# Kernel tuning notes

Measured on AMD Instinct MI355X. Metric: run time of the kernel, lower is better.

## Reference

```python
import jax, jax.numpy as jnp
import numpy as np

B, P, O, C = 32, 65536, 32, 2
THRESH = 0.35
VAR = (0.1, 0.2)
LOC_W, LANDM_W = 2.0, 1.0
ALPHA, GAMMA = 0.25, 1.5
EPS = 1e-7


def setup_inputs():
    key = jax.random.key(0)
    k = jax.random.split(key, 8)
    loc_data = jax.random.normal(k[0], (B, P, 4), jnp.float32) * 0.1
    conf_data = jax.random.normal(k[1], (B, P, C), jnp.float32)
    landm_data = jax.random.normal(k[2], (B, P, 10), jnp.float32) * 0.1
    # priors in center form (cx, cy, w, h)
    cxcy = jax.random.uniform(k[3], (P, 2), minval=0.05, maxval=0.95)
    wh = jax.random.uniform(k[4], (P, 2), minval=0.02, maxval=0.3)
    priors = jnp.concatenate([cxcy, wh], axis=-1).astype(jnp.float32)
    # targets [B, O, 15]: corner box (4) + 5 landmarks (10) + label (1, in {-1, +1})
    xy1 = jax.random.uniform(k[5], (B, O, 2), minval=0.0, maxval=0.7)
    bwh = jax.random.uniform(k[6], (B, O, 2), minval=0.05, maxval=0.25)
    boxes = jnp.concatenate([xy1, xy1 + bwh], axis=-1)
    landms = jnp.tile(xy1 + bwh * 0.5, (1, 1, 5))
    labels = (jax.random.randint(k[7], (B, O, 1), 0, 2) * 2 - 1).astype(jnp.float32)
    targets = jnp.concatenate([boxes, landms, labels], axis=-1)
    return {"loc_data": loc_data, "conf_data": conf_data, "landm_data": landm_data,
            "priors": priors, "targets": targets}


def point_form(pr):  # (cx,cy,w,h) -> (x1,y1,x2,y2)
    return jnp.concatenate([pr[:, :2] - pr[:, 2:] / 2, pr[:, :2] + pr[:, 2:] / 2], -1)


def pairwise_iou(a, b):  # a [O,4], b [P,4] corner form -> [O,P]
    lt = jnp.maximum(a[:, None, :2], b[None, :, :2])
    rb = jnp.minimum(a[:, None, 2:], b[None, :, 2:])
    whd = jnp.clip(rb - lt, 0.0)
    inter = whd[..., 0] * whd[..., 1]
    area_a = ((a[:, 2] - a[:, 0]) * (a[:, 3] - a[:, 1]))[:, None]
    area_b = ((b[:, 2] - b[:, 0]) * (b[:, 3] - b[:, 1]))[None, :]
    return inter / (area_a + area_b - inter)


def encode_landm(matched, priors):  # matched [P,10], priors [P,4] center form
    m = matched.reshape(P, 5, 2)
    g = (m - priors[:, None, :2]) / (VAR[0] * priors[:, None, 2:])
    return g.reshape(P, 10)


def match_one(truths, landms, labels, priors_pf, priors):
    ov = pairwise_iou(truths, priors_pf)                       # [O,P]
    best_prior_idx = jnp.argmax(ov, axis=1)                    # [O] best prior per gt
    best_truth_overlap = ov.max(axis=0)                        # [P]
    best_truth_idx = jnp.argmax(ov, axis=0)                    # [P]
    # ensure every gt keeps its best prior
    best_truth_overlap = best_truth_overlap.at[best_prior_idx].set(2.0)
    best_truth_idx = best_truth_idx.at[best_prior_idx].set(jnp.arange(truths.shape[0]))
    loc_t = truths[best_truth_idx]                             # [P,4] matched gt boxes (corner)
    conf = jnp.where(best_truth_overlap < THRESH, 0.0, labels[best_truth_idx])
    landm_t = encode_landm(landms[best_truth_idx], priors)     # [P,10]
    return loc_t, conf, landm_t


def decode(loc, priors):  # SSD center-form decode -> corner boxes
    xy = priors[..., :2] + loc[..., :2] * VAR[0] * priors[..., 2:]
    wh = priors[..., 2:] * jnp.exp(loc[..., 2:] * VAR[1])
    return jnp.concatenate([xy - wh / 2, xy + wh / 2], -1)


def giou(b1, b2):  # elementwise GIoU, corner form
    area1 = (b1[..., 2] - b1[..., 0]) * (b1[..., 3] - b1[..., 1])
    area2 = (b2[..., 2] - b2[..., 0]) * (b2[..., 3] - b2[..., 1])
    iw = jnp.clip(jnp.minimum(b1[..., 2], b2[..., 2]) - jnp.maximum(b1[..., 0], b2[..., 0]), 0.0)
    ih = jnp.clip(jnp.minimum(b1[..., 3], b2[..., 3]) - jnp.maximum(b1[..., 1], b2[..., 1]), 0.0)
    inter = iw * ih
    union = area1 + area2 - inter
    iou = inter / (union + EPS)
    ew = jnp.maximum(b1[..., 2], b2[..., 2]) - jnp.minimum(b1[..., 0], b2[..., 0])
    eh = jnp.maximum(b1[..., 3], b2[..., 3]) - jnp.minimum(b1[..., 1], b2[..., 1])
    enc = ew * eh
    return iou - (enc - union) / (enc + EPS)


def smooth_l1(x):
    ax = jnp.abs(x)
    return jnp.where(ax < 1.0, 0.5 * x * x, ax - 0.5)


def reference(loc_data, conf_data, landm_data, priors, targets):
    # matching uses detached (.data) priors/targets in the original
    priors_c = jax.lax.stop_gradient(priors)
    targets_c = jax.lax.stop_gradient(targets)
    truths, landms, labels = targets_c[..., :4], targets_c[..., 4:14], targets_c[..., 14]
    priors_pf = point_form(priors_c)
    loc_t, conf_raw, landm_t = jax.vmap(match_one, in_axes=(0, 0, 0, None, None))(
        truths, landms, labels, priors_pf, priors_c)  # [B,P,4],[B,P],[B,P,10]

    # landmark loss on pos1 = conf > 0 (label +1: face with landmarks)
    pos1 = conf_raw > 0
    N1 = jnp.maximum(pos1.sum().astype(jnp.float32), 1.0)
    loss_landm = (smooth_l1(landm_data - landm_t).sum(-1) * pos1).sum() * LANDM_W

    # loc GIoU loss on pos = conf != 0
    pos = conf_raw != 0
    conf_t = pos.astype(jnp.int32)  # conf_t[pos] = 1, background 0
    dec = decode(loc_data, priors_c[None])  # [B,P,4]
    loss_l = jnp.where(pos, 1.0 - giou(dec, loc_t), 0.0).sum() * LOC_W

    # focal loss over all B*P anchors (size_average=False -> sum)
    logp = jax.nn.log_softmax(conf_data, axis=-1)
    logp_t = jnp.take_along_axis(logp, conf_t[..., None], axis=-1)[..., 0]
    p_t = jnp.exp(logp_t)
    loss_c = (-ALPHA * (1.0 - p_t) ** GAMMA * logp_t).sum()

    # original normalizes loss_l and loss_c by num_pos_landm sum (N), landm by N1 (==N)
    N = N1
    return (loss_l / N, loss_c / N, loss_landm / N1)
```

## Files before the change

### kernel.cpp

```cpp
#include <hip/hip_runtime.h>
#include <cstdint>

#define B_ 32
#define P_ 65536
#define O_ 32
#define GX_ 64
#define KC_ 4
#define NCELL_ 16
#define NC_ (NCELL_ * NCELL_)
#define HB_ 32
#define PPH_ (P_ / (HB_ * 256))
#define MARGIN_ 0.1501f
#define THRESH_ 0.35f
#define VAR0 0.1f
#define VAR1 0.2f
#define EPS_ 1e-7f
#define ALPHA_ 0.25f

struct WSHdr {
  unsigned long long gkey[B_ * O_];
  float4 part[GX_ * B_];
  double corr[B_][4];
  unsigned blkcnt[HB_ * NC_];
  unsigned blkbase[HB_ * NC_];
  unsigned cellid[P_];
  unsigned idx_sorted[P_];
  float4 priors_sorted[P_];
};

__device__ __forceinline__ float frcp(float x) { return __builtin_amdgcn_rcpf(x); }

template <int CTRL>
__device__ __forceinline__ float dpp_fmax(float v) {
  int s = __builtin_amdgcn_update_dpp(0, __float_as_int(v), CTRL, 0xF, 0xF, true);
  return fmaxf(v, __int_as_float(s));
}
template <int CTRL>
__device__ __forceinline__ unsigned dpp_umax(unsigned v) {
  unsigned u = (unsigned)__builtin_amdgcn_update_dpp(0, (int)v, CTRL, 0xF, 0xF, true);
  return u > v ? u : v;
}

__device__ __forceinline__ float focal_term(float2 cf, bool pos) {
  float mx = fmaxf(cf.x, cf.y);
  float lse = mx + __logf(1.f + __expf(-fabsf(cf.x - cf.y)));
  float logpt = (pos ? cf.y : cf.x) - lse;
  float pt = __expf(logpt);
  float om = 1.f - pt;
  return -ALPHA_ * om * sqrtf(om) * logpt;
}

__device__ __forceinline__ float giou_term(float4 pr, float4 loc,
                                           float b2x1, float b2y1,
                                           float b2x2, float b2y2) {
  float dx = pr.x + loc.x * VAR0 * pr.z;
  float dy = pr.y + loc.y * VAR0 * pr.w;
  float dw = pr.z * __expf(loc.z * VAR1);
  float dh = pr.w * __expf(loc.w * VAR1);
  float b1x1 = dx - dw * 0.5f, b1y1 = dy - dh * 0.5f;
  float b1x2 = dx + dw * 0.5f, b1y2 = dy + dh * 0.5f;
  float a1 = (b1x2 - b1x1) * (b1y2 - b1y1);
  float a2 = (b2x2 - b2x1) * (b2y2 - b2y1);
  float iw = fmaxf(fminf(b1x2, b2x2) - fmaxf(b1x1, b2x1), 0.f);
  float ih = fmaxf(fminf(b1y2, b2y2) - fmaxf(b1y1, b2y1), 0.f);
  float inter = iw * ih;
  float uni = a1 + a2 - inter;
  float iou = inter * frcp(uni + EPS_);
  float ew = fmaxf(b1x2, b2x2) - fminf(b1x1, b2x1);
  float eh = fmaxf(b1y2, b2y2) - fminf(b1y1, b2y1);
  float enc = ew * eh;
  float g = iou - (enc - uni) * frcp(enc + EPS_);
  return 1.f - g;
}

__device__ __forceinline__ float landm_term(float4 pr,
                                            const float* __restrict__ lmrow,
                                            const float* __restrict__ tlm_row) {
  float rw = frcp(VAR0 * pr.z);
  float rh = frcp(VAR0 * pr.w);
  float llm = 0.f;
  #pragma unroll
  for (int q = 0; q < 5; ++q) {
    float2 d = *reinterpret_cast<const float2*>(lmrow + q * 2);
    float ex = d.x - (tlm_row[2 * q] - pr.x) * rw;
    float ey = d.y - (tlm_row[2 * q + 1] - pr.y) * rh;
    float ax = fabsf(ex), ay = fabsf(ey);
    llm += (ax < 1.f) ? 0.5f * ex * ex : ax - 0.5f;
    llm += (ay < 1.f) ? 0.5f * ey * ey : ay - 0.5f;
  }
  return llm;
}


__global__ __launch_bounds__(256) void k_init2(WSHdr* ws) {
  const int t = blockIdx.x * 256 + threadIdx.x;
  if (t < B_ * O_) ws->gkey[t] = 0xFFFFFFFFull;
}

__global__ __launch_bounds__(256) void k_hist(const float* __restrict__ priors,
                                              WSHdr* __restrict__ ws) {
  __shared__ unsigned lh[NC_];
  const int tid = threadIdx.x;
  lh[tid] = 0u;
  __syncthreads();
  const int pb0 = blockIdx.x * (256 * PPH_);
  #pragma unroll
  for (int i = 0; i < PPH_; ++i) {
    const int p = pb0 + i * 256 + tid;
    float4 pr = reinterpret_cast<const float4*>(priors)[p];
    int cx = min(NCELL_ - 1, max(0, (int)(pr.x * (float)NCELL_)));
    int cy = min(NCELL_ - 1, max(0, (int)(pr.y * (float)NCELL_)));
    unsigned c = (unsigned)(cy * NCELL_ + cx);
    ws->cellid[p] = c;
    atomicAdd(&lh[c], 1u);
  }
  __syncthreads();
  ws->blkcnt[blockIdx.x * NC_ + tid] = lh[tid];
}

__global__ __launch_bounds__(256) void k_scan2(WSHdr* ws) {
  __shared__ unsigned s[NC_];
  const int c = threadIdx.x;
  unsigned tot = 0;
  for (int blk = 0; blk < HB_; ++blk) tot += ws->blkcnt[blk * NC_ + c];
  s[c] = tot;
  __syncthreads();
  for (int off = 1; off < NC_; off <<= 1) {
    unsigned t = (c >= off) ? s[c - off] : 0u;
    __syncthreads();
    s[c] += t;
    __syncthreads();
  }
  unsigned run = s[c] - tot;
  for (int blk = 0; blk < HB_; ++blk) {
    ws->blkbase[blk * NC_ + c] = run;
    run += ws->blkcnt[blk * NC_ + c];
  }
}

__global__ __launch_bounds__(256) void k_scatter2(const float* __restrict__ priors,
                                                  WSHdr* __restrict__ ws) {
  __shared__ unsigned lcur[NC_];
  const int tid = threadIdx.x;
  lcur[tid] = ws->blkbase[blockIdx.x * NC_ + tid];
  __syncthreads();
  const int pb0 = blockIdx.x * (256 * PPH_);
  #pragma unroll
  for (int i = 0; i < PPH_; ++i) {
    const int p = pb0 + i * 256 + tid;
    unsigned c = ws->cellid[p];
    unsigned slot = atomicAdd(&lcur[c], 1u);
    ws->idx_sorted[slot] = (unsigned)p;
    ws->priors_sorted[slot] = reinterpret_cast<const float4*>(priors)[p];
  }
}

__global__ __launch_bounds__(256) void k_fused2(const float* __restrict__ loc_data,
                                                const float* __restrict__ conf_data,
                                                const float* __restrict__ landm_data,
                                                const float* __restrict__ targets,
                                                WSHdr* __restrict__ ws) {
  __shared__ float tsh[O_][4];
  __shared__ float tlbl[O_];
  __shared__ float tlm[O_][10];
  __shared__ unsigned long long kq[O_][17];
  __shared__ float4 wsum[4];
  const int b = blockIdx.y;
  const int tid = threadIdx.x;
  const int lane = tid & 63, wid = tid >> 6;
  if (tid < O_) {
    const float* trow = targets + ((size_t)b * O_ + tid) * 15;
    tsh[tid][0] = trow[0]; tsh[tid][1] = trow[1];
    tsh[tid][2] = trow[2]; tsh[tid][3] = trow[3];
    #pragma unroll
    for (int k = 0; k < 10; ++k) tlm[tid][k] = trow[4 + k];
    tlbl[tid] = trow[14];
  }
  for (int i = tid; i < O_ * 17; i += 256) ((unsigned long long*)kq)[i] = 0ull;
  __syncthreads();

  const int slot0 = blockIdx.x * 1024 + tid * KC_;
  float4 pr[KC_];
  float px1[KC_], py1[KC_], px2[KC_], py2[KC_], pa[KC_], bov[KC_];
  int bidx[KC_];
  unsigned pinv[KC_];
  uint4 opv = *reinterpret_cast<const uint4*>(&ws->idx_sorted[slot0]);
  pinv[0] = 0xFFFFFFFFu - opv.x; pinv[1] = 0xFFFFFFFFu - opv.y;
  pinv[2] = 0xFFFFFFFFu - opv.z; pinv[3] = 0xFFFFFFFFu - opv.w;
  float mnx = 1e9f, mxx = -1e9f, mny = 1e9f, mxy = -1e9f;
  #pragma unroll
  for (int k = 0; k < KC_; ++k) {
    pr[k] = ws->priors_sorted[slot0 + k];
    px1[k] = pr[k].x - pr[k].z * 0.5f; py1[k] = pr[k].y - pr[k].w * 0.5f;
    px2[k] = pr[k].x + pr[k].z * 0.5f; py2[k] = pr[k].y + pr[k].w * 0.5f;
    pa[k] = (px2[k] - px1[k]) * (py2[k] - py1[k]);
    bov[k] = 0.f; bidx[k] = 0;
    mnx = fminf(mnx, pr[k].x); mxx = fmaxf(mxx, pr[k].x);
    mny = fminf(mny, pr[k].y); mxy = fmaxf(mxy, pr[k].y);
  }
  #pragma unroll
  for (int i = 1; i < 64; i <<= 1) {
    mnx = fminf(mnx, __shfl_xor(mnx, i));
    mxx = fmaxf(mxx, __shfl_xor(mxx, i));
    mny = fminf(mny, __shfl_xor(mny, i));
    mxy = fmaxf(mxy, __shfl_xor(mxy, i));
  }

  const float* __restrict__ tb = targets + (size_t)b * O_ * 15;
  for (int o = 0; o < O_; ++o) {
    const float x1 = tb[o * 15 + 0], y1 = tb[o * 15 + 1];
    const float x2 = tb[o * 15 + 2], y2 = tb[o * 15 + 3];
    bool hit = (x1 - MARGIN_ <= mxx) && (x2 + MARGIN_ >= mnx) &&
               (y1 - MARGIN_ <= mxy) && (y2 + MARGIN_ >= mny);
    if (hit) {
      const float ta = (x2 - x1) * (y2 - y1);
      float tiou = 0.f;
      unsigned tinv = 0u;
      #pragma unroll
      for (int k = 0; k < KC_; ++k) {
        float iw = fmaxf(fminf(x2, px2[k]) - fmaxf(x1, px1[k]), 0.f);
        float ih = fmaxf(fminf(y2, py2[k]) - fmaxf(y1, py1[k]), 0.f);
        float inter = iw * ih;
        float iou = inter * frcp(ta + pa[k] - inter);
        if (iou > bov[k]) { bov[k] = iou; bidx[k] = o; }
        if (iou > tiou || (iou == tiou && pinv[k] > tinv)) {
          tiou = iou; tinv = pinv[k];
        }
      }
      float m = tiou;
      m = dpp_fmax<0x128>(m);
      m = dpp_fmax<0x124>(m);
      m = dpp_fmax<0x122>(m);
      m = dpp_fmax<0x121>(m);
      unsigned cand = (tiou == m) ? tinv : 0u;
      cand = dpp_umax<0x128>(cand);
      cand = dpp_umax<0x124>(cand);
      cand = dpp_umax<0x122>(cand);
      cand = dpp_umax<0x121>(cand);
      if ((lane & 15) == 0)
        kq[o][wid * 4 + (lane >> 4)] =
            ((unsigned long long)__float_as_uint(m) << 32) |
            (unsigned long long)cand;
    }
  }

  float vx = 0.f, vy = 0.f, vz = 0.f, vw = 0.f;
  #pragma unroll
  for (int k = 0; k < KC_; ++k) {
    const unsigned p = 0xFFFFFFFFu - pinv[k];
    const size_t bp = (size_t)b * P_ + p;
    const float ov = bov[k];
    const int idx = bidx[k];
    const bool pos = !(ov < THRESH_);
    const bool pos1 = pos && (tlbl[idx] > 0.f);
    float2 cf = reinterpret_cast<const float2*>(conf_data)[bp];
    vy += focal_term(cf, pos);
    if (pos) {
      float4 loc = reinterpret_cast<const float4*>(loc_data)[bp];
      vx += giou_term(pr[k], loc, tsh[idx][0], tsh[idx][1], tsh[idx][2], tsh[idx][3]);
      if (pos1) {
        vw += 1.f;
        vz += landm_term(pr[k], landm_data + bp * 10, &tlm[idx][0]);
      }
    }
  }

  __syncthreads();
  if (tid < O_) {
    unsigned long long best = kq[tid][0];
    #pragma unroll
    for (int s = 1; s < 16; ++s) {
      unsigned long long v = kq[tid][s];
      if (v > best) best = v;
    }
    atomicMax(&ws->gkey[(size_t)b * O_ + tid], best);
  }

  #pragma unroll
  for (int i = 32; i > 0; i >>= 1) {
    vx += __shfl_xor(vx, i);
    vy += __shfl_xor(vy, i);
    vz += __shfl_xor(vz, i);
    vw += __shfl_xor(vw, i);
  }
  if (lane == 0) wsum[wid] = make_float4(vx, vy, vz, vw);
  __syncthreads();
  if (tid == 0) {
    float sx = 0.f, sy = 0.f, sz = 0.f, sw = 0.f;
    #pragma unroll
    for (int w = 0; w < 4; ++w) {
      sx += wsum[w].x; sy += wsum[w].y; sz += wsum[w].z; sw += wsum[w].w;
    }
    ws->part[(size_t)blockIdx.y * GX_ + blockIdx.x] = make_float4(sx, sy, sz, sw);
  }
}

__global__ __launch_bounds__(64) void k_fix(const float* __restrict__ loc_data,
                                            const float* __restrict__ conf_data,
                                            const float* __restrict__ landm_data,
                                            const float* __restrict__ priors,
                                            const float* __restrict__ targets,
                                            WSHdr* __restrict__ ws) {
  __shared__ float tsh[O_][5];
  __shared__ float tlbl[O_];
  __shared__ float tlm[O_][10];
  const int b = blockIdx.x;
  const int tid = threadIdx.x;
  if (tid < O_) {
    const float* trow = targets + ((size_t)b * O_ + tid) * 15;
    float x1 = trow[0], y1 = trow[1], x2 = trow[2], y2 = trow[3];
    tsh[tid][0] = x1; tsh[tid][1] = y1; tsh[tid][2] = x2; tsh[tid][3] = y2;
    tsh[tid][4] = (x2 - x1) * (y2 - y1);
    #pragma unroll
    for (int k = 0; k < 10; ++k) tlm[tid][k] = trow[4 + k];
    tlbl[tid] = trow[14];
  }
  __syncthreads();

  unsigned fp = 0xFFFFFFFFu;
  if (tid < O_)
    fp = 0xFFFFFFFFu - (unsigned)(ws->gkey[(size_t)b * O_ + tid] & 0xFFFFFFFFull);
  bool alive = tid < O_;
  for (int j2 = 0; j2 < O_; ++j2) {
    unsigned f2 = __shfl(fp, j2, 64);
    if (j2 > tid && f2 == fp) alive = false;
  }

  float dll = 0.f, dlc = 0.f, dllm = 0.f, dn1 = 0.f;
  if (alive) {
    const int p = (int)fp;
    const size_t bp = (size_t)b * P_ + p;
    float4 pr = reinterpret_cast<const float4*>(priors)[p];
    float px1 = pr.x - pr.z * 0.5f, py1 = pr.y - pr.w * 0.5f;
    float px2 = pr.x + pr.z * 0.5f, py2 = pr.y + pr.w * 0.5f;
    float pa = (px2 - px1) * (py2 - py1);
    float bov = 0.f;
    int bidx = 0;
    for (int o = 0; o < O_; ++o) {
      const float x1 = tsh[o][0], y1 = tsh[o][1], x2 = tsh[o][2], y2 = tsh[o][3];
      const float ta = tsh[o][4];
      float iw = fmaxf(fminf(x2, px2) - fmaxf(x1, px1), 0.f);
      float ih = fmaxf(fminf(y2, py2) - fmaxf(y1, py1), 0.f);
      float inter = iw * ih;
      float iou = inter * frcp(ta + pa - inter);
      if (iou > bov) { bov = iou; bidx = o; }
    }
    float2 cf = reinterpret_cast<const float2*>(conf_data)[bp];
    float4 loc = reinterpret_cast<const float4*>(loc_data)[bp];
    const float* lmrow = landm_data + bp * 10;
    {
      const bool pos = !(bov < THRESH_);
      const bool pos1 = pos && (tlbl[bidx] > 0.f);
      dlc -= focal_term(cf, pos);
      if (pos) {
        dll -= giou_term(pr, loc, tsh[bidx][0], tsh[bidx][1], tsh[bidx][2], tsh[bidx][3]);
        if (pos1) {
          dn1 -= 1.f;
          dllm -= landm_term(pr, lmrow, &tlm[bidx][0]);
        }
      }
    }
    {
      const int idx = tid;
      const bool pos1 = tlbl[idx] > 0.f;
      dlc += focal_term(cf, true);
      dll += giou_term(pr, loc, tsh[idx][0], tsh[idx][1], tsh[idx][2], tsh[idx][3]);
      if (pos1) {
        dn1 += 1.f;
        dllm += landm_term(pr, lmrow, &tlm[idx][0]);
      }
    }
  }
  #pragma unroll
  for (int i = 32; i > 0; i >>= 1) {
    dll += __shfl_xor(dll, i);
    dlc += __shfl_xor(dlc, i);
    dllm += __shfl_xor(dllm, i);
    dn1 += __shfl_xor(dn1, i);
  }
  if (tid == 0) {
    ws->corr[b][0] = (double)dll;
    ws->corr[b][1] = (double)dlc;
    ws->corr[b][2] = (double)dllm;
    ws->corr[b][3] = (double)dn1;
  }
}

__global__ __launch_bounds__(256) void k_final(const WSHdr* __restrict__ ws,
                                               float* __restrict__ out) {
  __shared__ double sh[4][4];
  const int tid = threadIdx.x;
  double sx = 0.0, sy = 0.0, sz = 0.0, sw = 0.0;
  for (int i = tid; i < GX_ * B_; i += 256) {
    float4 v = ws->part[i];
    sx += v.x; sy += v.y; sz += v.z; sw += v.w;
  }
  if (tid < B_) {
    sx += ws->corr[tid][0];
    sy += ws->corr[tid][1];
    sz += ws->corr[tid][2];
    sw += ws->corr[tid][3];
  }
  #pragma unroll
  for (int i = 32; i > 0; i >>= 1) {
    sx += __shfl_xor(sx, i);
    sy += __shfl_xor(sy, i);
    sz += __shfl_xor(sz, i);
    sw += __shfl_xor(sw, i);
  }
  const int wave = tid >> 6, lane = tid & 63;
  if (lane == 0) { sh[wave][0] = sx; sh[wave][1] = sy; sh[wave][2] = sz; sh[wave][3] = sw; }
  __syncthreads();
  if (tid == 0) {
    double ax = 0, ay = 0, az = 0, aw = 0;
    #pragma unroll
    for (int w = 0; w < 4; ++w) { ax += sh[w][0]; ay += sh[w][1]; az += sh[w][2]; aw += sh[w][3]; }
    double n1 = aw < 1.0 ? 1.0 : aw;
    out[0] = (float)(2.0 * ax / n1);
    out[1] = (float)(ay / n1);
    out[2] = (float)(az / n1);
  }
}

extern "C" void kernel_launch(void* const* d_in, const int* in_sizes, int n_in,
                              void* d_out, int out_size, void* d_ws, size_t ws_size,
                              hipStream_t stream) {
  (void)in_sizes; (void)n_in; (void)out_size; (void)ws_size;
  const float* loc     = (const float*)d_in[0];
  const float* conf    = (const float*)d_in[1];
  const float* landm   = (const float*)d_in[2];
  const float* priors  = (const float*)d_in[3];
  const float* targets = (const float*)d_in[4];
  WSHdr* ws = (WSHdr*)d_ws;
  float* out = (float*)d_out;

  hipLaunchKernelGGL(k_init2, dim3(4), dim3(256), 0, stream, ws);
  hipLaunchKernelGGL(k_hist, dim3(HB_), dim3(256), 0, stream, priors, ws);
  hipLaunchKernelGGL(k_scan2, dim3(1), dim3(256), 0, stream, ws);
  hipLaunchKernelGGL(k_scatter2, dim3(HB_), dim3(256), 0, stream, priors, ws);
  hipLaunchKernelGGL(k_fused2, dim3(GX_, B_), dim3(256), 0, stream,
                     loc, conf, landm, targets, ws);
  hipLaunchKernelGGL(k_fix, dim3(B_), dim3(64), 0, stream,
                     loc, conf, landm, priors, targets, ws);
  hipLaunchKernelGGL(k_final, dim3(1), dim3(256), 0, stream, ws, out);
}
```

Measured before the change: 88.12 us.

## Split fused match/loss kernel so loss reads inputs in original coalesced order

The fused matching-and-loss kernel is split in two. The matching kernel now writes per-prior best IoU and index, packed into 32 bits, in sorted order. A new loss kernel walks priors in their original order, finding each result through a sortrank table, so the large loc, conf and landmark reads become coalesced instead of scattered gathers. The init kernel is folded into the histogram kernel to save a launch. The cost is an extra launch plus a B*P intermediate buffer that is written and read back, and the packing truncates the low 6 IoU bits.

Result: slower. 105.2 us (+19.3%).

```diff
diff --git a/kernel.cpp b/kernel.cpp
--- a/kernel.cpp
+++ b/kernel.cpp
@@ -23,8 +23,8 @@
   double corr[B_][4];
   unsigned blkcnt[HB_ * NC_];
   unsigned blkbase[HB_ * NC_];
-  unsigned cellid[P_];
   unsigned idx_sorted[P_];
+  unsigned sortrank[P_];
   float4 priors_sorted[P_];
 };
 
@@ -92,16 +92,15 @@
 }
 
 
-__global__ __launch_bounds__(256) void k_init2(WSHdr* ws) {
-  const int t = blockIdx.x * 256 + threadIdx.x;
-  if (t < B_ * O_) ws->gkey[t] = 0xFFFFFFFFull;
-}
-
 __global__ __launch_bounds__(256) void k_hist(const float* __restrict__ priors,
-                                              WSHdr* __restrict__ ws) {
+                                              WSHdr* __restrict__ ws,
+                                              unsigned* __restrict__ cellid) {
   __shared__ unsigned lh[NC_];
   const int tid = threadIdx.x;
   lh[tid] = 0u;
+  if (blockIdx.x == 0) {
+    for (int i = tid; i < B_ * O_; i += 256) ws->gkey[i] = 0xFFFFFFFFull;
+  }
   __syncthreads();
   const int pb0 = blockIdx.x * (256 * PPH_);
   #pragma unroll
@@ -111,7 +110,7 @@
     int cx = min(NCELL_ - 1, max(0, (int)(pr.x * (float)NCELL_)));
     int cy = min(NCELL_ - 1, max(0, (int)(pr.y * (float)NCELL_)));
     unsigned c = (unsigned)(cy * NCELL_ + cx);
-    ws->cellid[p] = c;
+    cellid[p] = c;
     atomicAdd(&lh[c], 1u);
   }
   __syncthreads();
@@ -139,7 +138,8 @@
 }
 
 __global__ __launch_bounds__(256) void k_scatter2(const float* __restrict__ priors,
-                                                  WSHdr* __restrict__ ws) {
+                                                  WSHdr* __restrict__ ws,
+                                                  const unsigned* __restrict__ cellid) {
   __shared__ unsigned lcur[NC_];
   const int tid = threadIdx.x;
   lcur[tid] = ws->blkbase[blockIdx.x * NC_ + tid];
@@ -148,39 +148,24 @@
   #pragma unroll
   for (int i = 0; i < PPH_; ++i) {
     const int p = pb0 + i * 256 + tid;
-    unsigned c = ws->cellid[p];
+    unsigned c = cellid[p];
     unsigned slot = atomicAdd(&lcur[c], 1u);
     ws->idx_sorted[slot] = (unsigned)p;
+    ws->sortrank[p] = slot;
     ws->priors_sorted[slot] = reinterpret_cast<const float4*>(priors)[p];
   }
 }
 
-__global__ __launch_bounds__(256) void k_fused2(const float* __restrict__ loc_data,
-                                                const float* __restrict__ conf_data,
-                                                const float* __restrict__ landm_data,
-                                                const float* __restrict__ targets,
-                                                WSHdr* __restrict__ ws) {
-  __shared__ float tsh[O_][4];
-  __shared__ float tlbl[O_];
-  __shared__ float tlm[O_][10];
+__global__ __launch_bounds__(256) void k_match2(const float* __restrict__ targets,
+                                                WSHdr* __restrict__ ws,
+                                                unsigned* __restrict__ pb32) {
   __shared__ unsigned long long kq[O_][17];
-  __shared__ float4 wsum[4];
   const int b = blockIdx.y;
   const int tid = threadIdx.x;
   const int lane = tid & 63, wid = tid >> 6;
-  if (tid < O_) {
-    const float* trow = targets + ((size_t)b * O_ + tid) * 15;
-    tsh[tid][0] = trow[0]; tsh[tid][1] = trow[1];
-    tsh[tid][2] = trow[2]; tsh[tid][3] = trow[3];
-    #pragma unroll
-    for (int k = 0; k < 10; ++k) tlm[tid][k] = trow[4 + k];
-    tlbl[tid] = trow[14];
-  }
   for (int i = tid; i < O_ * 17; i += 256) ((unsigned long long*)kq)[i] = 0ull;
-  __syncthreads();
 
   const int slot0 = blockIdx.x * 1024 + tid * KC_;
-  float4 pr[KC_];
   float px1[KC_], py1[KC_], px2[KC_], py2[KC_], pa[KC_], bov[KC_];
   int bidx[KC_];
   unsigned pinv[KC_];
@@ -190,13 +175,13 @@
   float mnx = 1e9f, mxx = -1e9f, mny = 1e9f, mxy = -1e9f;
   #pragma unroll
   for (int k = 0; k < KC_; ++k) {
-    pr[k] = ws->priors_sorted[slot0 + k];
-    px1[k] = pr[k].x - pr[k].z * 0.5f; py1[k] = pr[k].y - pr[k].w * 0.5f;
-    px2[k] = pr[k].x + pr[k].z * 0.5f; py2[k] = pr[k].y + pr[k].w * 0.5f;
+    float4 pr = ws->priors_sorted[slot0 + k];
+    px1[k] = pr.x - pr.z * 0.5f; py1[k] = pr.y - pr.w * 0.5f;
+    px2[k] = pr.x + pr.z * 0.5f; py2[k] = pr.y + pr.w * 0.5f;
     pa[k] = (px2[k] - px1[k]) * (py2[k] - py1[k]);
     bov[k] = 0.f; bidx[k] = 0;
-    mnx = fminf(mnx, pr[k].x); mxx = fmaxf(mxx, pr[k].x);
-    mny = fminf(mny, pr[k].y); mxy = fmaxf(mxy, pr[k].y);
+    mnx = fminf(mnx, pr.x); mxx = fmaxf(mxx, pr.x);
+    mny = fminf(mny, pr.y); mxy = fmaxf(mxy, pr.y);
   }
   #pragma unroll
   for (int i = 1; i < 64; i <<= 1) {
@@ -205,6 +190,7 @@
     mny = fminf(mny, __shfl_xor(mny, i));
     mxy = fmaxf(mxy, __shfl_xor(mxy, i));
   }
+  __syncthreads();
 
   const float* __restrict__ tb = targets + (size_t)b * O_ * 15;
   for (int o = 0; o < O_; ++o) {
@@ -244,26 +230,12 @@
     }
   }
 
-  float vx = 0.f, vy = 0.f, vz = 0.f, vw = 0.f;
-  #pragma unroll
-  for (int k = 0; k < KC_; ++k) {
-    const unsigned p = 0xFFFFFFFFu - pinv[k];
-    const size_t bp = (size_t)b * P_ + p;
-    const float ov = bov[k];
-    const int idx = bidx[k];
-    const bool pos = !(ov < THRESH_);
-    const bool pos1 = pos && (tlbl[idx] > 0.f);
-    float2 cf = reinterpret_cast<const float2*>(conf_data)[bp];
-    vy += focal_term(cf, pos);
-    if (pos) {
-      float4 loc = reinterpret_cast<const float4*>(loc_data)[bp];
-      vx += giou_term(pr[k], loc, tsh[idx][0], tsh[idx][1], tsh[idx][2], tsh[idx][3]);
-      if (pos1) {
-        vw += 1.f;
-        vz += landm_term(pr[k], landm_data + bp * 10, &tlm[idx][0]);
-      }
-    }
-  }
+  uint4 outv;
+  outv.x = (__float_as_uint(bov[0]) & 0xFFFFFFC0u) | (unsigned)bidx[0];
+  outv.y = (__float_as_uint(bov[1]) & 0xFFFFFFC0u) | (unsigned)bidx[1];
+  outv.z = (__float_as_uint(bov[2]) & 0xFFFFFFC0u) | (unsigned)bidx[2];
+  outv.w = (__float_as_uint(bov[3]) & 0xFFFFFFC0u) | (unsigned)bidx[3];
+  *reinterpret_cast<uint4*>(&pb32[(size_t)b * P_ + slot0]) = outv;
 
   __syncthreads();
   if (tid < O_) {
@@ -275,6 +247,53 @@
     }
     atomicMax(&ws->gkey[(size_t)b * O_ + tid], best);
   }
+}
+
+__global__ __launch_bounds__(256) void k_loss3(const float* __restrict__ loc_data,
+                                               const float* __restrict__ conf_data,
+                                               const float* __restrict__ landm_data,
+                                               const float* __restrict__ priors,
+                                               const float* __restrict__ targets,
+                                               WSHdr* __restrict__ ws,
+                                               const unsigned* __restrict__ pb32) {
+  __shared__ float tx1[O_], ty1[O_], tx2[O_], ty2[O_], tlbl[O_];
+  __shared__ float tlm[O_][10];
+  __shared__ float4 wsum[4];
+  const int b = blockIdx.y;
+  const int tid = threadIdx.x;
+  if (tid < O_) {
+    const float* trow = targets + ((size_t)b * O_ + tid) * 15;
+    tx1[tid] = trow[0]; ty1[tid] = trow[1]; tx2[tid] = trow[2]; ty2[tid] = trow[3];
+    #pragma unroll
+    for (int k = 0; k < 10; ++k) tlm[tid][k] = trow[4 + k];
+    tlbl[tid] = trow[14];
+  }
+  __syncthreads();
+
+  float vx = 0.f, vy = 0.f, vz = 0.f, vw = 0.f;
+  #pragma unroll
+  for (int k = 0; k < KC_; ++k) {
+    const unsigned p = (unsigned)((blockIdx.x * KC_ + k) * 256 + tid);
+    const size_t bp = (size_t)b * P_ + p;
+    const unsigned slot = ws->sortrank[p];
+    const unsigned v = pb32[(size_t)b * P_ + slot];
+    const float ov = __uint_as_float(v & 0xFFFFFFC0u);
+    const int idx = (int)(v & 0x3Fu);
+    const bool pos = !(ov < THRESH_);
+    const bool pos1 = pos && (tlbl[idx] > 0.f);
+
+    float2 cf = reinterpret_cast<const float2*>(conf_data)[bp];
+    vy += focal_term(cf, pos);
+    if (pos) {
+      float4 pr = reinterpret_cast<const float4*>(priors)[p];
+      float4 loc = reinterpret_cast<const float4*>(loc_data)[bp];
+      vx += giou_term(pr, loc, tx1[idx], ty1[idx], tx2[idx], ty2[idx]);
+      if (pos1) {
+        vw += 1.f;
+        vz += landm_term(pr, landm_data + bp * 10, &tlm[idx][0]);
+      }
+    }
+  }
 
   #pragma unroll
   for (int i = 32; i > 0; i >>= 1) {
@@ -283,7 +302,8 @@
     vz += __shfl_xor(vz, i);
     vw += __shfl_xor(vw, i);
   }
-  if (lane == 0) wsum[wid] = make_float4(vx, vy, vz, vw);
+  const int wave = tid >> 6, lane = tid & 63;
+  if (lane == 0) wsum[wave] = make_float4(vx, vy, vz, vw);
   __syncthreads();
   if (tid == 0) {
     float sx = 0.f, sy = 0.f, sz = 0.f, sw = 0.f;
@@ -349,7 +369,8 @@
     float4 loc = reinterpret_cast<const float4*>(loc_data)[bp];
     const float* lmrow = landm_data + bp * 10;
     {
-      const bool pos = !(bov < THRESH_);
+      const float ovt = __uint_as_float(__float_as_uint(bov) & 0xFFFFFFC0u);
+      const bool pos = !(ovt < THRESH_);
       const bool pos1 = pos && (tlbl[bidx] > 0.f);
       dlc -= focal_term(cf, pos);
       if (pos) {
@@ -432,14 +453,16 @@
   const float* priors  = (const float*)d_in[3];
   const float* targets = (const float*)d_in[4];
   WSHdr* ws = (WSHdr*)d_ws;
+  unsigned* aux = (unsigned*)((char*)d_ws + sizeof(WSHdr));
   float* out = (float*)d_out;
 
-  hipLaunchKernelGGL(k_init2, dim3(4), dim3(256), 0, stream, ws);
-  hipLaunchKernelGGL(k_hist, dim3(HB_), dim3(256), 0, stream, priors, ws);
+  hipLaunchKernelGGL(k_hist, dim3(HB_), dim3(256), 0, stream, priors, ws, aux);
   hipLaunchKernelGGL(k_scan2, dim3(1), dim3(256), 0, stream, ws);
-  hipLaunchKernelGGL(k_scatter2, dim3(HB_), dim3(256), 0, stream, priors, ws);
-  hipLaunchKernelGGL(k_fused2, dim3(GX_, B_), dim3(256), 0, stream,
-                     loc, conf, landm, targets, ws);
+  hipLaunchKernelGGL(k_scatter2, dim3(HB_), dim3(256), 0, stream, priors, ws, aux);
+  hipLaunchKernelGGL(k_match2, dim3(GX_, B_), dim3(256), 0, stream,
+                     targets, ws, aux);
+  hipLaunchKernelGGL(k_loss3, dim3(GX_, B_), dim3(256), 0, stream,
+                     loc, conf, landm, priors, targets, ws, aux);
   hipLaunchKernelGGL(k_fix, dim3(B_), dim3(64), 0, stream,
                      loc, conf, landm, priors, targets, ws);
   hipLaunchKernelGGL(k_final, dim3(1), dim3(256), 0, stream, ws, out);
```
